# Kernel optimization log

Measured on AMD Instinct MI355X. Metric: run time of the kernel, lower is better.

Reference implementation:

```python
import jax, jax.numpy as jnp
import numpy as np
from jax import lax


def setup_inputs() -> dict:
    key = jax.random.key(0)
    ks = jax.random.split(key, 13)
    B, L, H, E, V, T = 32, 256, 512, 512, 32000, 64
    s = 0.05
    return {
        "z": jax.random.normal(ks[0], (B, L), jnp.float32),
        "embedding": jax.random.normal(ks[1], (V, E), jnp.float32) * s,
        "Wh": jax.random.normal(ks[2], (H, L), jnp.float32) * s,
        "bh": jax.random.normal(ks[3], (H,), jnp.float32) * s,
        "Wc": jax.random.normal(ks[4], (H, L), jnp.float32) * s,
        "bc": jax.random.normal(ks[5], (H,), jnp.float32) * s,
        "Wih": jax.random.normal(ks[6], (4 * H, E), jnp.float32) * s,
        "Whh": jax.random.normal(ks[7], (4 * H, H), jnp.float32) * s,
        "bih": jax.random.normal(ks[8], (4 * H,), jnp.float32) * s,
        "bhh": jax.random.normal(ks[9], (4 * H,), jnp.float32) * s,
        "Wfc": jax.random.normal(ks[10], (V, H), jnp.float32) * s,
        "bfc": jax.random.normal(ks[11], (V,), jnp.float32) * s,
        "context_length": T,
    }


def reference(z, embedding, Wh, bh, Wc, bc, Wih, Whh, bih, bhh, Wfc, bfc, context_length):
    # project latent to initial LSTM state: [B, H]
    h0 = z @ Wh.T + bh
    c0 = z @ Wc.T + bc
    b_gates = bih + bhh

    def step(carry, _):
        h, c, x = carry  # each [B, H] / [B, E]
        gates = x @ Wih.T + h @ Whh.T + b_gates  # [B, 4H] (pytorch gate order i,f,g,o)
        i, f, g, o = jnp.split(gates, 4, axis=-1)
        c_new = jax.nn.sigmoid(f) * c + jax.nn.sigmoid(i) * jnp.tanh(g)
        h_new = jax.nn.sigmoid(o) * jnp.tanh(c_new)
        logits = h_new @ Wfc.T + bfc  # [B, V]
        pred = jnp.argmax(logits, axis=-1)  # greedy token
        x_new = embedding[pred]  # [B, E]
        return (h_new, c_new, x_new), logits

    # first step feeds h itself as the input (x is None in torch code)
    _, logits = lax.scan(step, (h0, c0, h0), None, length=context_length)
    return jnp.transpose(logits, (1, 0, 2))  # [B, T, V]
```

## Files before the change

kernel.cpp:

```cpp
#include <hip/hip_runtime.h>
#include <hip/hip_bf16.h>
#include <cstdint>
#include <cstddef>

#define NB 32
#define NL 256
#define NH 512
#define NE 512
#define NV 32000
#define NT 64
#define NJ 2048
#define NK 1024
#define NKT 16

typedef __attribute__((ext_vector_type(8))) short bf16x8;
typedef __attribute__((ext_vector_type(4))) float f32x4;


__device__ __forceinline__ unsigned int sortable_f32(float f) {
  unsigned int s = __float_as_uint(f);
  return (s & 0x80000000u) ? ~s : (s | 0x80000000u);
}

__device__ __forceinline__ unsigned long long pack_key(float f, int v) {
  return ((unsigned long long)sortable_f32(f) << 32) |
         (unsigned long long)(unsigned int)(~v);
}

__device__ __forceinline__ unsigned long long shfl_xor_u64(unsigned long long x, int m) {
  unsigned int lo = (unsigned int)x;
  unsigned int hi = (unsigned int)(x >> 32);
  lo = __shfl_xor(lo, m, 64);
  hi = __shfl_xor(hi, m, 64);
  return ((unsigned long long)hi << 32) | lo;
}

__device__ __forceinline__ uint32_t pack_hi16(uint32_t u0, uint32_t u1) {
  return __builtin_amdgcn_perm(u1, u0, 0x07060302u);
}

__device__ __forceinline__ void split3(float4 wa, float4 wb,
                                       bf16x8& A1, bf16x8& A2, bf16x8& A3) {
  union U { uint32_t w[4]; bf16x8 v; };
  U u1, u2, u3;
  float e[8] = {wa.x, wa.y, wa.z, wa.w, wb.x, wb.y, wb.z, wb.w};
#pragma unroll
  for (int p = 0; p < 4; ++p) {
    float e0 = e[2 * p], e1 = e[2 * p + 1];
    uint32_t a0 = __float_as_uint(e0), a1 = __float_as_uint(e1);
    u1.w[p] = pack_hi16(a0, a1);
    float r0 = e0 - __uint_as_float(a0 & 0xffff0000u);
    float r1 = e1 - __uint_as_float(a1 & 0xffff0000u);
    uint32_t b0 = __float_as_uint(r0), b1 = __float_as_uint(r1);
    u2.w[p] = pack_hi16(b0, b1);
    float q0 = r0 - __uint_as_float(b0 & 0xffff0000u);
    float q1 = r1 - __uint_as_float(b1 & 0xffff0000u);
    u3.w[p] = pack_hi16(__float_as_uint(q0), __float_as_uint(q1));
  }
  A1 = u1.v; A2 = u2.v; A3 = u3.v;
}

__device__ __forceinline__ unsigned long long load_key(const unsigned long long* p) {
  return __hip_atomic_load(p, __ATOMIC_ACQUIRE, __HIP_MEMORY_SCOPE_AGENT);
}


__global__ void k_init(const float* __restrict__ z, const float* __restrict__ Wh,
                       const float* __restrict__ bh, const float* __restrict__ Wc,
                       const float* __restrict__ bc, float* __restrict__ hbuf,
                       float* __restrict__ cbuf, unsigned long long* __restrict__ keys) {
  int idx = blockIdx.x * 256 + threadIdx.x;
  int b = idx >> 9, hh = idx & 511;
  const float* zr  = z + b * NL;
  const float* whr = Wh + hh * NL;
  const float* wcr = Wc + hh * NL;
  float ah = 0.f, ac = 0.f;
  for (int k = 0; k < NL; ++k) {
    float zv = zr[k];
    ah += zv * whr[k];
    ac += zv * wcr[k];
  }
  hbuf[b * NH + hh] = ah + bh[hh];
  cbuf[b * NH + hh] = ac + bc[hh];
  if (idx < 64)
    __hip_atomic_store(&keys[idx], 0ULL, __ATOMIC_RELEASE, __HIP_MEMORY_SCOPE_AGENT);
}

__global__ void k_transposeW(const float* __restrict__ Wih, const float* __restrict__ Whh,
                             float* __restrict__ WT) {
  __shared__ float tile[32][33];
  int j0 = blockIdx.x * 32;
  int k0 = blockIdx.y * 32;
  int tx = threadIdx.x & 31;
  int ty = threadIdx.x >> 5;
  for (int r = ty; r < 32; r += 8) {
    int j = j0 + r, k = k0 + tx;
    tile[r][tx] = (k < NE) ? Wih[j * NE + k] : Whh[j * NH + (k - NE)];
  }
  __syncthreads();
  for (int r = ty; r < 32; r += 8) {
    int k = k0 + r, j = j0 + tx;
    WT[(size_t)k * NJ + j] = tile[tx][r];
  }
}

__global__ void k_packWfc(const float* __restrict__ Wfc, unsigned short* __restrict__ Wpk) {
  int bid = blockIdx.x;
  int tid = threadIdx.x;
  int lane = tid & 63, wv = tid >> 6;
  int r16 = lane & 15, g = lane >> 4;
  const float* wr = Wfc + (size_t)(bid * 16 + r16) * NH + g * 8;
#pragma unroll
  for (int q = 0; q < 4; ++q) {
    int kq = wv * 4 + q;
    float4 wa = *(const float4*)(wr + kq * 32);
    float4 wb = *(const float4*)(wr + kq * 32 + 4);
    bf16x8 A1, A2, A3;
    split3(wa, wb, A1, A2, A3);
    size_t base = ((size_t)(bid * 16 + kq) * 3) << 9;
    *(bf16x8*)(Wpk + base + lane * 8) = A1;
    *(bf16x8*)(Wpk + base + 512 + lane * 8) = A2;
    *(bf16x8*)(Wpk + base + 1024 + lane * 8) = A3;
  }
}

__global__ void k_gates(const float* __restrict__ WT, const float* __restrict__ emb,
                        const float* __restrict__ hbuf, const unsigned long long* __restrict__ keys,
                        float* __restrict__ partials, int step) {
  __shared__ unsigned int spred[NB];
  int tid  = threadIdx.x;
  int jthr = tid & 31, bthr = tid >> 5;
  int j0 = blockIdx.x * 128 + jthr * 4;
  int k0 = blockIdx.y * 64;
  int b0 = bthr * 4;
  const float* hin = hbuf + (size_t)(step & 1) * NB * NH;
  const bool isx = (k0 < NE);

  if (step > 0 && isx && tid < NB) {
    unsigned long long key = load_key(&keys[((step - 1) & 1) * NB + tid]);
    unsigned int pred = ~(unsigned int)(key & 0xFFFFFFFFu);
    if (pred >= NV) pred = 0;
    spred[tid] = pred;
  }
  __syncthreads();

  const float* xp[4];
#pragma unroll
  for (int i = 0; i < 4; ++i) {
    int b = b0 + i;
    if (!isx) {
      xp[i] = hin + (size_t)b * NH - NE;
    } else if (step == 0) {
      xp[i] = hin + (size_t)b * NE;
    } else {
      xp[i] = emb + (size_t)spred[b] * NE;
    }
  }

  float acc[4][4];
#pragma unroll
  for (int jj = 0; jj < 4; ++jj)
#pragma unroll
    for (int i = 0; i < 4; ++i) acc[jj][i] = 0.f;

#pragma unroll 4
  for (int k = k0; k < k0 + 64; ++k) {
    float4 w = *(const float4*)(WT + (size_t)k * NJ + j0);
#pragma unroll
    for (int i = 0; i < 4; ++i) {
      float xv = xp[i][k];
      acc[0][i] += w.x * xv;
      acc[1][i] += w.y * xv;
      acc[2][i] += w.z * xv;
      acc[3][i] += w.w * xv;
    }
  }

  int kt = blockIdx.y;
#pragma unroll
  for (int jj = 0; jj < 4; ++jj)
#pragma unroll
    for (int i = 0; i < 4; ++i)
      partials[((size_t)(j0 + jj) * NB + (b0 + i)) * NKT + kt] = acc[jj][i];
}

__global__ void k_cell(const float* __restrict__ partials, const float* __restrict__ bih,
                       const float* __restrict__ bhh, float* __restrict__ hbuf,
                       float* __restrict__ cbuf, unsigned short* __restrict__ hs,
                       unsigned long long* __restrict__ keys, int step) {
  int idx = blockIdx.x * 256 + threadIdx.x;
  int b = idx >> 9, hh = idx & 511;
  float g4[4];
#pragma unroll
  for (int g = 0; g < 4; ++g) {
    int j = g * NH + hh;
    const float4* p4 = (const float4*)(partials + ((size_t)j * NB + b) * NKT);
    float4 a0 = p4[0], a1 = p4[1], a2 = p4[2], a3 = p4[3];
    float s = ((a0.x + a0.y) + (a0.z + a0.w)) + ((a1.x + a1.y) + (a1.z + a1.w)) +
              ((a2.x + a2.y) + (a2.z + a2.w)) + ((a3.x + a3.y) + (a3.z + a3.w));
    g4[g] = s + bih[j] + bhh[j];
  }
  float ig = 1.0f / (1.0f + expf(-g4[0]));
  float fg = 1.0f / (1.0f + expf(-g4[1]));
  float gg = tanhf(g4[2]);
  float og = 1.0f / (1.0f + expf(-g4[3]));
  float c  = cbuf[b * NH + hh];
  float cn = fg * c + ig * gg;
  float hn = og * tanhf(cn);
  cbuf[b * NH + hh] = cn;
  hbuf[(size_t)((step + 1) & 1) * NB * NH + b * NH + hh] = hn;

  uint32_t u = __float_as_uint(hn);
  float r1 = hn - __uint_as_float(u & 0xffff0000u);
  uint32_t u2 = __float_as_uint(r1);
  float r2 = r1 - __uint_as_float(u2 & 0xffff0000u);
  uint32_t u3 = __float_as_uint(r2);
  hs[0 * NB * NH + b * NH + hh] = (unsigned short)(u >> 16);
  hs[1 * NB * NH + b * NH + hh] = (unsigned short)(u2 >> 16);
  hs[2 * NB * NH + b * NH + hh] = (unsigned short)(u3 >> 16);

  if (idx < NB)
    __hip_atomic_store(&keys[(step & 1) * NB + idx], 0ULL,
                       __ATOMIC_RELEASE, __HIP_MEMORY_SCOPE_AGENT);
}

__global__ __launch_bounds__(512, 1) void k_logits3(
    const unsigned short* __restrict__ Wpk, const float* __restrict__ bfc,
    const unsigned short* __restrict__ hs, float* __restrict__ out,
    unsigned long long* __restrict__ keys, int step) {
  __shared__ __align__(16) unsigned short H[3][32][520];
  __shared__ __align__(16) float tbuf[32][132];
  __shared__ unsigned long long kmax[32];

  const int tid = threadIdx.x, bid = blockIdx.x;
  const int lane = tid & 63, wid = tid >> 6;
  const int r16 = lane & 15, g = lane >> 4;

  const int wg = bid * 8 + wid;
  const unsigned short* wbase = Wpk + (((size_t)wg * 48) << 9) + lane * 8;

  bf16x8 Acur[3], Anx[3];
#pragma unroll
  for (int s = 0; s < 3; ++s) Acur[s] = *(const bf16x8*)(wbase + ((0 * 3 + s) << 9));
#pragma unroll
  for (int s = 0; s < 3; ++s) Anx[s] = *(const bf16x8*)(wbase + ((1 * 3 + s) << 9));

#pragma unroll
  for (int i = 0; i < 12; ++i) {
    int idx = tid + i * 512;
    int s = idx >> 11, rem = idx & 2047;
    int row = rem >> 6, ch = rem & 63;
    float4 d = *(const float4*)(hs + (size_t)s * (NB * NH) + row * NH + ch * 8);
    *(float4*)(&H[s][row][ch * 8]) = d;
  }
  if (tid < 32) kmax[tid] = 0ULL;
  __syncthreads();

  f32x4 acc0 = {0.f, 0.f, 0.f, 0.f};
  f32x4 acc1 = {0.f, 0.f, 0.f, 0.f};

#pragma unroll
  for (int kq = 0; kq < 16; ++kq) {
    bf16x8 An2[3];
    if (kq < 14) {
#pragma unroll
      for (int s = 0; s < 3; ++s)
        An2[s] = *(const bf16x8*)(wbase + (((kq + 2) * 3 + s) << 9));
    }
    const int ko = kq * 32 + g * 8;
    bf16x8 B1n0 = *(const bf16x8*)(&H[0][r16][ko]);
    bf16x8 B1n1 = *(const bf16x8*)(&H[0][r16 + 16][ko]);
    bf16x8 B2n0 = *(const bf16x8*)(&H[1][r16][ko]);
    bf16x8 B2n1 = *(const bf16x8*)(&H[1][r16 + 16][ko]);
    bf16x8 B3n0 = *(const bf16x8*)(&H[2][r16][ko]);
    bf16x8 B3n1 = *(const bf16x8*)(&H[2][r16 + 16][ko]);

    acc0 = __builtin_amdgcn_mfma_f32_16x16x32_bf16(Acur[0], B1n0, acc0, 0, 0, 0);
    acc0 = __builtin_amdgcn_mfma_f32_16x16x32_bf16(Acur[0], B2n0, acc0, 0, 0, 0);
    acc0 = __builtin_amdgcn_mfma_f32_16x16x32_bf16(Acur[1], B1n0, acc0, 0, 0, 0);
    acc0 = __builtin_amdgcn_mfma_f32_16x16x32_bf16(Acur[1], B2n0, acc0, 0, 0, 0);
    acc0 = __builtin_amdgcn_mfma_f32_16x16x32_bf16(Acur[0], B3n0, acc0, 0, 0, 0);
    acc0 = __builtin_amdgcn_mfma_f32_16x16x32_bf16(Acur[2], B1n0, acc0, 0, 0, 0);

    acc1 = __builtin_amdgcn_mfma_f32_16x16x32_bf16(Acur[0], B1n1, acc1, 0, 0, 0);
    acc1 = __builtin_amdgcn_mfma_f32_16x16x32_bf16(Acur[0], B2n1, acc1, 0, 0, 0);
    acc1 = __builtin_amdgcn_mfma_f32_16x16x32_bf16(Acur[1], B1n1, acc1, 0, 0, 0);
    acc1 = __builtin_amdgcn_mfma_f32_16x16x32_bf16(Acur[1], B2n1, acc1, 0, 0, 0);
    acc1 = __builtin_amdgcn_mfma_f32_16x16x32_bf16(Acur[0], B3n1, acc1, 0, 0, 0);
    acc1 = __builtin_amdgcn_mfma_f32_16x16x32_bf16(Acur[2], B1n1, acc1, 0, 0, 0);

#pragma unroll
    for (int s = 0; s < 3; ++s) { Acur[s] = Anx[s]; Anx[s] = An2[s]; }
  }

  const int vwave = bid * 128 + wid * 16;
  float4 bv = *(const float4*)(bfc + vwave + g * 4);
  float lg0[4], lg1[4];
  unsigned long long key0 = 0ULL, key1 = 0ULL;
#pragma unroll
  for (int reg = 0; reg < 4; ++reg) {
    int v = vwave + 4 * g + reg;
    float bvr = (reg == 0) ? bv.x : (reg == 1) ? bv.y : (reg == 2) ? bv.z : bv.w;
    lg0[reg] = acc0[reg] + bvr;
    lg1[reg] = acc1[reg] + bvr;
    unsigned long long p0 = pack_key(lg0[reg], v);
    unsigned long long p1 = pack_key(lg1[reg], v);
    key0 = (p0 > key0) ? p0 : key0;
    key1 = (p1 > key1) ? p1 : key1;
  }
#pragma unroll
  for (int m = 16; m <= 32; m <<= 1) {
    unsigned long long o0 = shfl_xor_u64(key0, m);
    unsigned long long o1 = shfl_xor_u64(key1, m);
    key0 = (o0 > key0) ? o0 : key0;
    key1 = (o1 > key1) ? o1 : key1;
  }
  if (g == 0) {
    atomicMax(&kmax[r16], key0);
    atomicMax(&kmax[r16 + 16], key1);
  }
  __syncthreads();

#pragma unroll
  for (int reg = 0; reg < 4; ++reg) {
    int vloc = wid * 16 + 4 * g + reg;
    tbuf[r16][vloc] = lg0[reg];
    tbuf[r16 + 16][vloc] = lg1[reg];
  }
  __syncthreads();

  {
    int bb = tid >> 4, seg = tid & 15;
    f32x4 p0 = *(const f32x4*)(&tbuf[bb][seg * 8]);
    f32x4 p1 = *(const f32x4*)(&tbuf[bb][seg * 8 + 4]);
    float* dst = out + ((size_t)bb * NT + step) * NV + bid * 128 + seg * 8;
    __builtin_nontemporal_store(p0, (f32x4*)dst);
    __builtin_nontemporal_store(p1, (f32x4*)(dst + 4));
  }
  if (tid < 32) atomicMax(&keys[(step & 1) * NB + tid], kmax[tid]);
}


extern "C" void kernel_launch(void* const* d_in, const int* in_sizes, int n_in,
                              void* d_out, int out_size, void* d_ws, size_t ws_size,
                              hipStream_t stream) {
  (void)in_sizes; (void)n_in; (void)out_size; (void)ws_size;
  const float* z   = (const float*)d_in[0];
  const float* emb = (const float*)d_in[1];
  const float* Wh  = (const float*)d_in[2];
  const float* bh  = (const float*)d_in[3];
  const float* Wc  = (const float*)d_in[4];
  const float* bc  = (const float*)d_in[5];
  const float* Wih = (const float*)d_in[6];
  const float* Whh = (const float*)d_in[7];
  const float* bih = (const float*)d_in[8];
  const float* bhh = (const float*)d_in[9];
  const float* Wfc = (const float*)d_in[10];
  const float* bfc = (const float*)d_in[11];
  float* out = (float*)d_out;

  float* ws = (float*)d_ws;
  float* WT       = ws;
  float* partials = ws + 2097152;
  float* hbuf     = ws + 3145728;
  float* cbuf     = ws + 3178496;
  unsigned long long* keys = (unsigned long long*)(ws + 3194880);
  unsigned short* hs = (unsigned short*)(ws + 3195008);
  unsigned short* Wpk = (unsigned short*)(ws + 3219584);

  k_init<<<64, 256, 0, stream>>>(z, Wh, bh, Wc, bc, hbuf, cbuf, keys);
  k_transposeW<<<dim3(64, 32), 256, 0, stream>>>(Wih, Whh, WT);
  k_packWfc<<<2000, 256, 0, stream>>>(Wfc, Wpk);

  for (int t = 0; t < NT; ++t) {
    k_gates<<<dim3(16, 16), 256, 0, stream>>>(WT, emb, hbuf, keys, partials, t);
    k_cell<<<64, 256, 0, stream>>>(partials, bih, bhh, hbuf, cbuf, hs, keys, t);
    k_logits3<<<250, 512, 0, stream>>>(Wpk, bfc, hs, out, keys, t);
  }
}
```

Measured before the change: 3.026 ms.

## Fuse LSTM gate matvec and cell update into one per-step kernel

Replaces the split-K gates kernel and the separate cell kernel with a single kernel. In it, each thread computes all four gate dot products for one (batch, hidden) pair, reading the untransposed Wih/Whh rows directly. This removes the pre-transpose of the weights, the partials buffer round-trip through global memory and one kernel launch per step. The trade-off is much less parallelism per step: 128 blocks of 128 threads, each thread running a serial 1024-long reduction. That may expose load latency and leave many compute units idle.

Result: slower. 5.738 ms (+89.6%).

```diff
diff --git a/kernel.cpp b/kernel.cpp
--- a/kernel.cpp
+++ b/kernel.cpp
@@ -9,9 +9,6 @@
 #define NE 512
 #define NV 32000
 #define NT 64
-#define NJ 2048
-#define NK 1024
-#define NKT 16
 
 typedef __attribute__((ext_vector_type(8))) short bf16x8;
 typedef __attribute__((ext_vector_type(4))) float f32x4;
@@ -86,24 +83,6 @@
     __hip_atomic_store(&keys[idx], 0ULL, __ATOMIC_RELEASE, __HIP_MEMORY_SCOPE_AGENT);
 }
 
-__global__ void k_transposeW(const float* __restrict__ Wih, const float* __restrict__ Whh,
-                             float* __restrict__ WT) {
-  __shared__ float tile[32][33];
-  int j0 = blockIdx.x * 32;
-  int k0 = blockIdx.y * 32;
-  int tx = threadIdx.x & 31;
-  int ty = threadIdx.x >> 5;
-  for (int r = ty; r < 32; r += 8) {
-    int j = j0 + r, k = k0 + tx;
-    tile[r][tx] = (k < NE) ? Wih[j * NE + k] : Whh[j * NH + (k - NE)];
-  }
-  __syncthreads();
-  for (int r = ty; r < 32; r += 8) {
-    int k = k0 + r, j = j0 + tx;
-    WT[(size_t)k * NJ + j] = tile[tx][r];
-  }
-}
-
 __global__ void k_packWfc(const float* __restrict__ Wfc, unsigned short* __restrict__ Wpk) {
   int bid = blockIdx.x;
   int tid = threadIdx.x;
@@ -124,19 +103,20 @@
   }
 }
 
-__global__ void k_gates(const float* __restrict__ WT, const float* __restrict__ emb,
-                        const float* __restrict__ hbuf, const unsigned long long* __restrict__ keys,
-                        float* __restrict__ partials, int step) {
+__global__ __launch_bounds__(128) void k_gatescell(
+    const float* __restrict__ Wih, const float* __restrict__ Whh,
+    const float* __restrict__ emb, const float* __restrict__ bih,
+    const float* __restrict__ bhh, float* __restrict__ hbuf,
+    float* __restrict__ cbuf, unsigned short* __restrict__ hs,
+    unsigned long long* __restrict__ keys, int step) {
   __shared__ unsigned int spred[NB];
-  int tid  = threadIdx.x;
-  int jthr = tid & 31, bthr = tid >> 5;
-  int j0 = blockIdx.x * 128 + jthr * 4;
-  int k0 = blockIdx.y * 64;
-  int b0 = bthr * 4;
-  const float* hin = hbuf + (size_t)(step & 1) * NB * NH;
-  const bool isx = (k0 < NE);
-
-  if (step > 0 && isx && tid < NB) {
+  const int tid = threadIdx.x;
+  const int b = tid >> 2, hl = tid & 3;
+  const int hh = blockIdx.x * 4 + hl;
+  float* hbase = hbuf;
+  const float* hin = hbase + (size_t)(step & 1) * NB * NH;
+
+  if (step > 0 && tid < NB) {
     unsigned long long key = load_key(&keys[((step - 1) & 1) * NB + tid]);
     unsigned int pred = ~(unsigned int)(key & 0xFFFFFFFFu);
     if (pred >= NV) pred = 0;
@@ -144,61 +124,53 @@
   }
   __syncthreads();
 
-  const float* xp[4];
-#pragma unroll
-  for (int i = 0; i < 4; ++i) {
-    int b = b0 + i;
-    if (!isx) {
-      xp[i] = hin + (size_t)b * NH - NE;
-    } else if (step == 0) {
-      xp[i] = hin + (size_t)b * NE;
-    } else {
-      xp[i] = emb + (size_t)spred[b] * NE;
+  const float* xrow = (step == 0) ? (hin + (size_t)b * NE)
+                                  : (emb + (size_t)spred[b] * NE);
+  const float* hrow = hin + (size_t)b * NH;
+
+  const float* wx[4];
+  const float* wh[4];
+#pragma unroll
+  for (int g = 0; g < 4; ++g) {
+    wx[g] = Wih + (size_t)(g * NH + hh) * NE;
+    wh[g] = Whh + (size_t)(g * NH + hh) * NH;
+  }
+
+  float p[4][16];
+#pragma unroll
+  for (int kt = 0; kt < 16; ++kt) {
+    const bool isx = (kt < 8);
+    const float* xs = isx ? xrow : (hrow - NE);
+    const float* w0p = isx ? wx[0] : (wh[0] - NE);
+    const float* w1p = isx ? wx[1] : (wh[1] - NE);
+    const float* w2p = isx ? wx[2] : (wh[2] - NE);
+    const float* w3p = isx ? wx[3] : (wh[3] - NE);
+    float a0 = 0.f, a1 = 0.f, a2 = 0.f, a3 = 0.f;
+#pragma unroll 4
+    for (int q = 0; q < 16; ++q) {
+      int k = kt * 64 + q * 4;
+      float4 xv = *(const float4*)(xs + k);
+      float4 w0 = *(const float4*)(w0p + k);
+      float4 w1 = *(const float4*)(w1p + k);
+      float4 w2 = *(const float4*)(w2p + k);
+      float4 w3 = *(const float4*)(w3p + k);
+      a0 += w0.x * xv.x; a0 += w0.y * xv.y; a0 += w0.z * xv.z; a0 += w0.w * xv.w;
+      a1 += w1.x * xv.x; a1 += w1.y * xv.y; a1 += w1.z * xv.z; a1 += w1.w * xv.w;
+      a2 += w2.x * xv.x; a2 += w2.y * xv.y; a2 += w2.z * xv.z; a2 += w2.w * xv.w;
+      a3 += w3.x * xv.x; a3 += w3.y * xv.y; a3 += w3.z * xv.z; a3 += w3.w * xv.w;
     }
-  }
-
-  float acc[4][4];
-#pragma unroll
-  for (int jj = 0; jj < 4; ++jj)
-#pragma unroll
-    for (int i = 0; i < 4; ++i) acc[jj][i] = 0.f;
-
-#pragma unroll 4
-  for (int k = k0; k < k0 + 64; ++k) {
-    float4 w = *(const float4*)(WT + (size_t)k * NJ + j0);
-#pragma unroll
-    for (int i = 0; i < 4; ++i) {
-      float xv = xp[i][k];
-      acc[0][i] += w.x * xv;
-      acc[1][i] += w.y * xv;
-      acc[2][i] += w.z * xv;
-      acc[3][i] += w.w * xv;
-    }
-  }
-
-  int kt = blockIdx.y;
-#pragma unroll
-  for (int jj = 0; jj < 4; ++jj)
-#pragma unroll
-    for (int i = 0; i < 4; ++i)
-      partials[((size_t)(j0 + jj) * NB + (b0 + i)) * NKT + kt] = acc[jj][i];
-}
-
-__global__ void k_cell(const float* __restrict__ partials, const float* __restrict__ bih,
-                       const float* __restrict__ bhh, float* __restrict__ hbuf,
-                       float* __restrict__ cbuf, unsigned short* __restrict__ hs,
-                       unsigned long long* __restrict__ keys, int step) {
-  int idx = blockIdx.x * 256 + threadIdx.x;
-  int b = idx >> 9, hh = idx & 511;
+    p[0][kt] = a0; p[1][kt] = a1; p[2][kt] = a2; p[3][kt] = a3;
+  }
+
   float g4[4];
 #pragma unroll
   for (int g = 0; g < 4; ++g) {
+    float t0 = (p[g][0] + p[g][1]) + (p[g][2] + p[g][3]);
+    float t1 = (p[g][4] + p[g][5]) + (p[g][6] + p[g][7]);
+    float t2 = (p[g][8] + p[g][9]) + (p[g][10] + p[g][11]);
+    float t3 = (p[g][12] + p[g][13]) + (p[g][14] + p[g][15]);
     int j = g * NH + hh;
-    const float4* p4 = (const float4*)(partials + ((size_t)j * NB + b) * NKT);
-    float4 a0 = p4[0], a1 = p4[1], a2 = p4[2], a3 = p4[3];
-    float s = ((a0.x + a0.y) + (a0.z + a0.w)) + ((a1.x + a1.y) + (a1.z + a1.w)) +
-              ((a2.x + a2.y) + (a2.z + a2.w)) + ((a3.x + a3.y) + (a3.z + a3.w));
-    g4[g] = s + bih[j] + bhh[j];
+    g4[g] = (((t0 + t1) + t2) + t3) + bih[j] + bhh[j];
   }
   float ig = 1.0f / (1.0f + expf(-g4[0]));
   float fg = 1.0f / (1.0f + expf(-g4[1]));
@@ -208,7 +180,7 @@
   float cn = fg * c + ig * gg;
   float hn = og * tanhf(cn);
   cbuf[b * NH + hh] = cn;
-  hbuf[(size_t)((step + 1) & 1) * NB * NH + b * NH + hh] = hn;
+  hbase[(size_t)((step + 1) & 1) * NB * NH + b * NH + hh] = hn;
 
   uint32_t u = __float_as_uint(hn);
   float r1 = hn - __uint_as_float(u & 0xffff0000u);
@@ -219,8 +191,8 @@
   hs[1 * NB * NH + b * NH + hh] = (unsigned short)(u2 >> 16);
   hs[2 * NB * NH + b * NH + hh] = (unsigned short)(u3 >> 16);
 
-  if (idx < NB)
-    __hip_atomic_store(&keys[(step & 1) * NB + idx], 0ULL,
+  if (blockIdx.x == 0 && tid < NB)
+    __hip_atomic_store(&keys[(step & 1) * NB + tid], 0ULL,
                        __ATOMIC_RELEASE, __HIP_MEMORY_SCOPE_AGENT);
 }
 
@@ -360,21 +332,18 @@
   float* out = (float*)d_out;
 
   float* ws = (float*)d_ws;
-  float* WT       = ws;
-  float* partials = ws + 2097152;
-  float* hbuf     = ws + 3145728;
-  float* cbuf     = ws + 3178496;
-  unsigned long long* keys = (unsigned long long*)(ws + 3194880);
-  unsigned short* hs = (unsigned short*)(ws + 3195008);
-  unsigned short* Wpk = (unsigned short*)(ws + 3219584);
+  float* hbuf = ws;
+  float* cbuf = ws + 32768;
+  unsigned long long* keys = (unsigned long long*)(ws + 49152);
+  unsigned short* hs = (unsigned short*)(ws + 49280);
+  unsigned short* Wpk = (unsigned short*)(ws + 73856);
 
   k_init<<<64, 256, 0, stream>>>(z, Wh, bh, Wc, bc, hbuf, cbuf, keys);
-  k_transposeW<<<dim3(64, 32), 256, 0, stream>>>(Wih, Whh, WT);
   k_packWfc<<<2000, 256, 0, stream>>>(Wfc, Wpk);
 
   for (int t = 0; t < NT; ++t) {
-    k_gates<<<dim3(16, 16), 256, 0, stream>>>(WT, emb, hbuf, keys, partials, t);
-    k_cell<<<64, 256, 0, stream>>>(partials, bih, bhh, hbuf, cbuf, hs, keys, t);
+    k_gatescell<<<128, 128, 0, stream>>>(Wih, Whh, emb, bih, bhh,
+                                         hbuf, cbuf, hs, keys, t);
     k_logits3<<<250, 512, 0, stream>>>(Wpk, bfc, hs, out, keys, t);
   }
 }
```
